# Kernel tuning notes

Measured on AMD Instinct MI355X. Metric: run time of the kernel, lower is better.

The kernel has to match this reference:

```python
import jax, jax.numpy as jnp
import numpy as np

N = 100000   # nodes
E = 5000000  # edges (avg degree 50)
H = 16       # hidden dim


def gcn_conv(x, edge_index, edge_weight, W, b, num_nodes):
    """PyG GCNConv with edge weights: add self-loops (weight 1), symmetric
    normalization deg^-1/2 * w * deg^-1/2, linear transform, scatter-add."""
    row, col = edge_index[0], edge_index[1]  # source j -> target i
    loop = jnp.arange(num_nodes, dtype=edge_index.dtype)
    row = jnp.concatenate([row, loop])
    col = jnp.concatenate([col, loop])
    w = jnp.concatenate([edge_weight, jnp.ones((num_nodes,), edge_weight.dtype)])
    deg = jax.ops.segment_sum(w, col, num_segments=num_nodes)
    dinv = jnp.where(deg > 0, jax.lax.rsqrt(jnp.where(deg > 0, deg, 1.0)), 0.0)
    norm = dinv[row] * w * dinv[col]               # [E+N]
    h = x @ W                                      # [N, out]
    msg = norm[:, None] * h[row]                   # gather + scale
    out = jax.ops.segment_sum(msg, col, num_segments=num_nodes)  # scatter-add
    return out + b


def setup_inputs() -> dict:
    key = jax.random.key(0)
    k = jax.random.split(key, 7)
    x = jax.random.normal(k[0], (N, 1), dtype=jnp.float32)
    edge_index = jax.random.randint(k[1], (2, E), 0, N, dtype=jnp.int32)
    edge_attr = jax.random.uniform(k[2], (E,), dtype=jnp.float32)
    W1 = jax.random.normal(k[3], (1, H), dtype=jnp.float32) * (1.0 / np.sqrt(1.0))
    b1 = jnp.zeros((H,), dtype=jnp.float32)
    W2 = jax.random.normal(k[4], (H, 1), dtype=jnp.float32) * (1.0 / np.sqrt(H))
    b2 = jnp.zeros((1,), dtype=jnp.float32)
    return {"x": x, "edge_index": edge_index, "edge_attr": edge_attr,
            "W1": W1, "b1": b1, "W2": W2, "b2": b2}


def reference(x, edge_index, edge_attr, W1, b1, W2, b2):
    h = gcn_conv(x, edge_index, edge_attr, W1, b1, N)
    h = jax.nn.relu(h)
    out = gcn_conv(h, edge_index, edge_attr, W2, b2, N)
    return out
```

## Files before the change

kernel.cpp:

```cpp
#include <hip/hip_runtime.h>

#define T       256
#define BSHIFT  12
#define BSIZE   4096
#define MAXNB   32
#define M       32
#define EPB     4096
#define EPT     (EPB / T)

__global__ void k_count(const int* __restrict__ col, int* __restrict__ cntT,
                        int E, int nb, int ebp) {
    __shared__ int hist[MAXNB];
    int t = threadIdx.x, g = blockIdx.x;
    if (t < MAXNB) hist[t] = 0;
    __syncthreads();
    int base = g * EPB;
    bool full = (base + EPB <= E);
    if (full) {
#pragma unroll
        for (int k = 0; k < EPT / 4; ++k) {
            int4 c = *(const int4*)(col + base + (t + k * T) * 4);
            atomicAdd(&hist[c.x >> BSHIFT], 1);
            atomicAdd(&hist[c.y >> BSHIFT], 1);
            atomicAdd(&hist[c.z >> BSHIFT], 1);
            atomicAdd(&hist[c.w >> BSHIFT], 1);
        }
    } else {
        for (int k = 0; k < EPT; ++k) {
            int e = base + t + k * T;
            if (e < E) atomicAdd(&hist[col[e] >> BSHIFT], 1);
        }
    }
    __syncthreads();
    if (t < nb) cntT[t * ebp + g] = hist[t];
}

__global__ void k_scan(const int* __restrict__ cntT, int* __restrict__ ofsT,
                       int* __restrict__ tot, int eb, int ebp) {
    __shared__ int tsum[T];
    __shared__ int carry;
    int b = blockIdx.x, t = threadIdx.x;
    if (t == 0) carry = 0;
    __syncthreads();
    int rounds = (eb + T - 1) / T;
    for (int jr = 0; jr < rounds; ++jr) {
        int idx = jr * T + t;
        int v = (idx < eb) ? cntT[b * ebp + idx] : 0;
        tsum[t] = v;
        __syncthreads();
        for (int d = 1; d < T; d <<= 1) {
            int o = (t >= d) ? tsum[t - d] : 0;
            __syncthreads();
            tsum[t] += o;
            __syncthreads();
        }
        int excl = tsum[t] - v + carry;
        if (idx < eb) ofsT[b * ebp + idx] = excl;
        __syncthreads();
        if (t == 0) carry += tsum[T - 1];
        __syncthreads();
    }
    if (t == 0) tot[b] = carry;
}

__global__ void k_scatter(const int* __restrict__ row, const int* __restrict__ col,
                          const float* __restrict__ w,
                          const int* __restrict__ cntT, const int* __restrict__ ofsT,
                          const int* __restrict__ tot,
                          int2* __restrict__ rec, int E, int nb, int ebp) {
    __shared__ int  lofs[MAXNB + 1];
    __shared__ int  rnk[MAXNB];
    __shared__ int  rbase[MAXNB];
    __shared__ int2 buf[EPB];
    __shared__ unsigned char bkt[EPB];
    int t = threadIdx.x, g = blockIdx.x;
    if (t < MAXNB) rnk[t] = 0;
    if (t < 64) {
        int tv = (t < nb) ? ((tot[t] + 3) & ~3) : 0;
        int incA = tv;
#pragma unroll
        for (int d = 1; d < 32; d <<= 1) {
            int o = __shfl_up(incA, d, 64);
            if (t >= d) incA += o;
        }
        int h = (t < nb) ? cntT[t * ebp + g] : 0;
        int incB = h;
#pragma unroll
        for (int d = 1; d < 32; d <<= 1) {
            int o = __shfl_up(incB, d, 64);
            if (t >= d) incB += o;
        }
        if (t == 0) lofs[0] = 0;
        if (t < nb) {
            lofs[t + 1] = incB;
            rbase[t] = (incA - tv) + ofsT[t * ebp + g];
        }
    }
    __syncthreads();

    int base = g * EPB;
    bool full = (base + EPB <= E);
    if (full) {
#pragma unroll
        for (int k = 0; k < EPT / 4; ++k) {
            int idx = base + (t + k * T) * 4;
            int4   c  = *(const int4*)(col + idx);
            int4   r  = *(const int4*)(row + idx);
            float4 wv = *(const float4*)(w + idx);
            int b, rk, pos;
            b = c.x >> BSHIFT; rk = atomicAdd(&rnk[b], 1); pos = lofs[b] + rk;
            buf[pos] = make_int2(((c.x & (BSIZE-1)) << 17) | r.x, __float_as_int(wv.x));
            bkt[pos] = (unsigned char)b;
            b = c.y >> BSHIFT; rk = atomicAdd(&rnk[b], 1); pos = lofs[b] + rk;
            buf[pos] = make_int2(((c.y & (BSIZE-1)) << 17) | r.y, __float_as_int(wv.y));
            bkt[pos] = (unsigned char)b;
            b = c.z >> BSHIFT; rk = atomicAdd(&rnk[b], 1); pos = lofs[b] + rk;
            buf[pos] = make_int2(((c.z & (BSIZE-1)) << 17) | r.z, __float_as_int(wv.z));
            bkt[pos] = (unsigned char)b;
            b = c.w >> BSHIFT; rk = atomicAdd(&rnk[b], 1); pos = lofs[b] + rk;
            buf[pos] = make_int2(((c.w & (BSIZE-1)) << 17) | r.w, __float_as_int(wv.w));
            bkt[pos] = (unsigned char)b;
        }
    } else {
        for (int k = 0; k < EPT; ++k) {
            int e = base + t + k * T;
            if (e < E) {
                int c = col[e];
                int b = c >> BSHIFT;
                int rk = atomicAdd(&rnk[b], 1);
                int pos = lofs[b] + rk;
                buf[pos] = make_int2(((c & (BSIZE-1)) << 17) | row[e], __float_as_int(w[e]));
                bkt[pos] = (unsigned char)b;
            }
        }
    }
    __syncthreads();
    int total = lofs[nb];
    for (int j = t; j < total; j += T) {
        int b = bkt[j];
        rec[rbase[b] + (j - lofs[b])] = buf[j];
    }
}

template <bool HAS_SRC>
__global__ void k_acc(const int2* __restrict__ rec, const int* __restrict__ tot,
                      const float* __restrict__ src, float* __restrict__ part, int nb) {
    __shared__ float acc[BSIZE];
    __shared__ int   bst[MAXNB];
    int t = threadIdx.x, g = blockIdx.x;
    int b = g / M, m = g % M;
    if (t < 64) {
        int tv = (t < nb) ? ((tot[t] + 3) & ~3) : 0;
        int inc = tv;
#pragma unroll
        for (int d = 1; d < 32; d <<= 1) {
            int o = __shfl_up(inc, d, 64);
            if (t >= d) inc += o;
        }
        if (t < nb) bst[t] = inc - tv;
    }
    for (int j = t; j < BSIZE; j += T) acc[j] = 0.0f;
    __syncthreads();
    int s  = bst[b];
    int tb = tot[b];
    int chunk = ((tb + M - 1) / M + 7) & ~7;
    int lo = s + m * chunk;
    int hi = min(s + tb, lo + chunk);
    const int4* rec4 = (const int4*)rec;
    int i = lo + t * 8;
    for (; i + 7 < hi; i += T * 8) {
        int4 q0 = rec4[(i >> 1) + 0];
        int4 q1 = rec4[(i >> 1) + 1];
        int4 q2 = rec4[(i >> 1) + 2];
        int4 q3 = rec4[(i >> 1) + 3];
        float v0 = __int_as_float(q0.y), v1 = __int_as_float(q0.w);
        float v2 = __int_as_float(q1.y), v3 = __int_as_float(q1.w);
        float v4 = __int_as_float(q2.y), v5 = __int_as_float(q2.w);
        float v6 = __int_as_float(q3.y), v7 = __int_as_float(q3.w);
        if (HAS_SRC) {
            v0 *= src[q0.x & 0x1FFFF]; v1 *= src[q0.z & 0x1FFFF];
            v2 *= src[q1.x & 0x1FFFF]; v3 *= src[q1.z & 0x1FFFF];
            v4 *= src[q2.x & 0x1FFFF]; v5 *= src[q2.z & 0x1FFFF];
            v6 *= src[q3.x & 0x1FFFF]; v7 *= src[q3.z & 0x1FFFF];
        }
        atomicAdd(&acc[((unsigned)q0.x) >> 17], v0);
        atomicAdd(&acc[((unsigned)q0.z) >> 17], v1);
        atomicAdd(&acc[((unsigned)q1.x) >> 17], v2);
        atomicAdd(&acc[((unsigned)q1.z) >> 17], v3);
        atomicAdd(&acc[((unsigned)q2.x) >> 17], v4);
        atomicAdd(&acc[((unsigned)q2.z) >> 17], v5);
        atomicAdd(&acc[((unsigned)q3.x) >> 17], v6);
        atomicAdd(&acc[((unsigned)q3.z) >> 17], v7);
    }
    for (; i < hi; ++i) {
        int2 r = rec[i];
        float v = __int_as_float(r.y);
        if (HAS_SRC) v *= src[r.x & 0x1FFFF];
        atomicAdd(&acc[((unsigned)r.x) >> 17], v);
    }
    __syncthreads();
    float* dst = part + (size_t)g * BSIZE;
    for (int j = t; j < BSIZE; j += T) dst[j] = acc[j];
}

__device__ __forceinline__ float reduceM(const float* __restrict__ part, int n) {
    int b = n >> BSHIFT, o = n & (BSIZE - 1);
    const float* pp = part + (size_t)b * M * BSIZE + o;
    float s = 0.0f;
#pragma unroll
    for (int m = 0; m < M; ++m) s += pp[(size_t)m * BSIZE];
    return s;
}

__global__ void k_red_dinv(const float* __restrict__ part, const float* __restrict__ x,
                           float* __restrict__ dinv, float* __restrict__ p, int N) {
    int i = blockIdx.x * blockDim.x + threadIdx.x;
    if (i < N) {
        float d  = reduceM(part, i) + 1.0f;
        float di = rsqrtf(d);
        dinv[i] = di;
        p[i] = di * x[i];
    }
}

__global__ void k_red_mlp(const float* __restrict__ part, const float* __restrict__ dinv,
                          const float* __restrict__ p,
                          const float* __restrict__ W1, const float* __restrict__ b1,
                          const float* __restrict__ W2,
                          float* __restrict__ q, int N) {
    int i = blockIdx.x * blockDim.x + threadIdx.x;
    if (i < N) {
        float di = dinv[i];
        float s  = di * reduceM(part, i) + di * p[i];
        float acc = 0.0f;
#pragma unroll
        for (int k = 0; k < 16; ++k) {
            float h = fmaxf(s * W1[k] + b1[k], 0.0f);
            acc += h * W2[k];
        }
        q[i] = di * acc;
    }
}

__global__ void k_red_out(const float* __restrict__ part, const float* __restrict__ dinv,
                          const float* __restrict__ q, const float* __restrict__ b2,
                          float* __restrict__ out, int N) {
    int i = blockIdx.x * blockDim.x + threadIdx.x;
    if (i < N) {
        float di = dinv[i];
        out[i] = di * reduceM(part, i) + di * q[i] + b2[0];
    }
}

extern "C" void kernel_launch(void* const* d_in, const int* in_sizes, int n_in,
                              void* d_out, int out_size, void* d_ws, size_t ws_size,
                              hipStream_t stream) {
    const float* x  = (const float*)d_in[0];
    const int*   ei = (const int*)  d_in[1];
    const float* ew = (const float*)d_in[2];
    const float* W1 = (const float*)d_in[3];
    const float* b1 = (const float*)d_in[4];
    const float* W2 = (const float*)d_in[5];
    const float* b2 = (const float*)d_in[6];

    const int N = in_sizes[0];
    const int E = in_sizes[2];
    const int* row = ei;
    const int* col = ei + E;
    const int nb  = (N + BSIZE - 1) >> BSHIFT;
    const int eb  = (E + EPB - 1) / EPB;
    const int ebp = (eb + 63) & ~63;

    char* wsp = (char*)d_ws;
    auto take = [&](size_t bytes) {
        char* r = wsp; wsp += (bytes + 255) & ~(size_t)255; return (void*)r;
    };
    int2*  rec  = (int2*) take((size_t)(E + 4 * MAXNB) * 8);
    float* part = (float*)take((size_t)nb * M * BSIZE * 4);
    float* dinv = (float*)take((size_t)N * 4);
    float* p    = (float*)take((size_t)N * 4);
    float* q    = (float*)take((size_t)N * 4);
    int*   cntT = (int*)  take((size_t)MAXNB * ebp * 4);
    int*   ofsT = (int*)  take((size_t)MAXNB * ebp * 4);
    int*   tot  = (int*)  take(MAXNB * 4);

    float* out = (float*)d_out;

    const int nbk = (N + T - 1) / T;
    const int ab  = nb * M;

    k_count  <<<eb, T, 0, stream>>>(col, cntT, E, nb, ebp);
    k_scan   <<<nb, T, 0, stream>>>(cntT, ofsT, tot, eb, ebp);
    k_scatter<<<eb, T, 0, stream>>>(row, col, ew, cntT, ofsT, tot, rec, E, nb, ebp);

    k_acc<false><<<ab, T, 0, stream>>>(rec, tot, nullptr, part, nb);
    k_red_dinv  <<<nbk, T, 0, stream>>>(part, x, dinv, p, N);

    k_acc<true><<<ab, T, 0, stream>>>(rec, tot, p, part, nb);
    k_red_mlp  <<<nbk, T, 0, stream>>>(part, dinv, p, W1, b1, W2, q, N);

    k_acc<true><<<ab, T, 0, stream>>>(rec, tot, q, part, nb);
    k_red_out  <<<nbk, T, 0, stream>>>(part, dinv, q, b2, out, N);
}
```

Baseline: 239.1 us.

## Use nontemporal loads/stores, warp-shuffle scan, vectorized zeroing, retune M and EPB

Marks streaming global loads and stores (edge arrays, bucketed records, partial sums) as nontemporal, swaps the shared-memory block scan for a wave-shuffle scan, and vectorizes accumulator zeroing and writeback. It also doubles the per-bucket split M and halves edges per scatter block to raise parallelism, and adds launch bounds. The larger M doubles the partial buffer and the per-node reduction work in the reduce kernels. The nontemporal hints may also hurt when the records are re-read by both accumulation passes.

After: 268.9 us. +12.5%, slower.

```diff
diff --git a/kernel.cpp b/kernel.cpp
--- a/kernel.cpp
+++ b/kernel.cpp
@@ -4,12 +4,17 @@
 #define BSHIFT  12
 #define BSIZE   4096
 #define MAXNB   32
-#define M       32
-#define EPB     4096
+#define M       64
+#define EPB     2048
 #define EPT     (EPB / T)
 
-__global__ void k_count(const int* __restrict__ col, int* __restrict__ cntT,
-                        int E, int nb, int ebp) {
+typedef int   i4 __attribute__((ext_vector_type(4)));
+typedef int   i2v __attribute__((ext_vector_type(2)));
+typedef float f4 __attribute__((ext_vector_type(4)));
+
+__global__ __launch_bounds__(T) void k_count(const int* __restrict__ col,
+                                             int* __restrict__ cntT,
+                                             int E, int nb, int ebp) {
     __shared__ int hist[MAXNB];
     int t = threadIdx.x, g = blockIdx.x;
     if (t < MAXNB) hist[t] = 0;
@@ -19,7 +24,7 @@
     if (full) {
 #pragma unroll
         for (int k = 0; k < EPT / 4; ++k) {
-            int4 c = *(const int4*)(col + base + (t + k * T) * 4);
+            i4 c = __builtin_nontemporal_load((const i4*)(col + base + (t + k * T) * 4));
             atomicAdd(&hist[c.x >> BSHIFT], 1);
             atomicAdd(&hist[c.y >> BSHIFT], 1);
             atomicAdd(&hist[c.z >> BSHIFT], 1);
@@ -35,43 +40,46 @@
     if (t < nb) cntT[t * ebp + g] = hist[t];
 }
 
-__global__ void k_scan(const int* __restrict__ cntT, int* __restrict__ ofsT,
-                       int* __restrict__ tot, int eb, int ebp) {
-    __shared__ int tsum[T];
+__global__ __launch_bounds__(T) void k_scan(const int* __restrict__ cntT,
+                                            int* __restrict__ ofsT,
+                                            int* __restrict__ tot, int eb, int ebp) {
+    __shared__ int wsum[4];
     __shared__ int carry;
-    int b = blockIdx.x, t = threadIdx.x;
+    int b = blockIdx.x, t = threadIdx.x, lane = t & 63, wid = t >> 6;
     if (t == 0) carry = 0;
     __syncthreads();
     int rounds = (eb + T - 1) / T;
     for (int jr = 0; jr < rounds; ++jr) {
         int idx = jr * T + t;
         int v = (idx < eb) ? cntT[b * ebp + idx] : 0;
-        tsum[t] = v;
+        int inc = v;
+#pragma unroll
+        for (int d = 1; d < 64; d <<= 1) {
+            int o = __shfl_up(inc, d, 64);
+            if (lane >= d) inc += o;
+        }
+        if (lane == 63) wsum[wid] = inc;
         __syncthreads();
-        for (int d = 1; d < T; d <<= 1) {
-            int o = (t >= d) ? tsum[t - d] : 0;
-            __syncthreads();
-            tsum[t] += o;
-            __syncthreads();
-        }
-        int excl = tsum[t] - v + carry;
-        if (idx < eb) ofsT[b * ebp + idx] = excl;
+        int add = carry;
+        for (int w = 0; w < wid; ++w) add += wsum[w];
+        if (idx < eb) ofsT[b * ebp + idx] = inc - v + add;
         __syncthreads();
-        if (t == 0) carry += tsum[T - 1];
+        if (t == 0) carry += wsum[0] + wsum[1] + wsum[2] + wsum[3];
         __syncthreads();
     }
     if (t == 0) tot[b] = carry;
 }
 
-__global__ void k_scatter(const int* __restrict__ row, const int* __restrict__ col,
-                          const float* __restrict__ w,
-                          const int* __restrict__ cntT, const int* __restrict__ ofsT,
-                          const int* __restrict__ tot,
-                          int2* __restrict__ rec, int E, int nb, int ebp) {
+__global__ __launch_bounds__(T) void k_scatter(
+        const int* __restrict__ row, const int* __restrict__ col,
+        const float* __restrict__ w,
+        const int* __restrict__ cntT, const int* __restrict__ ofsT,
+        const int* __restrict__ tot,
+        i2v* __restrict__ rec, int E, int nb, int ebp) {
     __shared__ int  lofs[MAXNB + 1];
     __shared__ int  rnk[MAXNB];
     __shared__ int  rbase[MAXNB];
-    __shared__ int2 buf[EPB];
+    __shared__ i2v  buf[EPB];
     __shared__ unsigned char bkt[EPB];
     int t = threadIdx.x, g = blockIdx.x;
     if (t < MAXNB) rnk[t] = 0;
@@ -104,22 +112,23 @@
 #pragma unroll
         for (int k = 0; k < EPT / 4; ++k) {
             int idx = base + (t + k * T) * 4;
-            int4   c  = *(const int4*)(col + idx);
-            int4   r  = *(const int4*)(row + idx);
-            float4 wv = *(const float4*)(w + idx);
+            i4 c  = __builtin_nontemporal_load((const i4*)(col + idx));
+            i4 r  = __builtin_nontemporal_load((const i4*)(row + idx));
+            f4 wv = __builtin_nontemporal_load((const f4*)(w + idx));
             int b, rk, pos;
+            i2v v;
             b = c.x >> BSHIFT; rk = atomicAdd(&rnk[b], 1); pos = lofs[b] + rk;
-            buf[pos] = make_int2(((c.x & (BSIZE-1)) << 17) | r.x, __float_as_int(wv.x));
-            bkt[pos] = (unsigned char)b;
+            v.x = ((c.x & (BSIZE-1)) << 17) | r.x; v.y = __float_as_int(wv.x);
+            buf[pos] = v; bkt[pos] = (unsigned char)b;
             b = c.y >> BSHIFT; rk = atomicAdd(&rnk[b], 1); pos = lofs[b] + rk;
-            buf[pos] = make_int2(((c.y & (BSIZE-1)) << 17) | r.y, __float_as_int(wv.y));
-            bkt[pos] = (unsigned char)b;
+            v.x = ((c.y & (BSIZE-1)) << 17) | r.y; v.y = __float_as_int(wv.y);
+            buf[pos] = v; bkt[pos] = (unsigned char)b;
             b = c.z >> BSHIFT; rk = atomicAdd(&rnk[b], 1); pos = lofs[b] + rk;
-            buf[pos] = make_int2(((c.z & (BSIZE-1)) << 17) | r.z, __float_as_int(wv.z));
-            bkt[pos] = (unsigned char)b;
+            v.x = ((c.z & (BSIZE-1)) << 17) | r.z; v.y = __float_as_int(wv.z);
+            buf[pos] = v; bkt[pos] = (unsigned char)b;
             b = c.w >> BSHIFT; rk = atomicAdd(&rnk[b], 1); pos = lofs[b] + rk;
-            buf[pos] = make_int2(((c.w & (BSIZE-1)) << 17) | r.w, __float_as_int(wv.w));
-            bkt[pos] = (unsigned char)b;
+            v.x = ((c.w & (BSIZE-1)) << 17) | r.w; v.y = __float_as_int(wv.w);
+            buf[pos] = v; bkt[pos] = (unsigned char)b;
         }
     } else {
         for (int k = 0; k < EPT; ++k) {
@@ -129,8 +138,10 @@
                 int b = c >> BSHIFT;
                 int rk = atomicAdd(&rnk[b], 1);
                 int pos = lofs[b] + rk;
-                buf[pos] = make_int2(((c & (BSIZE-1)) << 17) | row[e], __float_as_int(w[e]));
-                bkt[pos] = (unsigned char)b;
+                i2v v;
+                v.x = ((c & (BSIZE-1)) << 17) | row[e];
+                v.y = __float_as_int(w[e]);
+                buf[pos] = v; bkt[pos] = (unsigned char)b;
             }
         }
     }
@@ -138,13 +149,14 @@
     int total = lofs[nb];
     for (int j = t; j < total; j += T) {
         int b = bkt[j];
-        rec[rbase[b] + (j - lofs[b])] = buf[j];
+        __builtin_nontemporal_store(buf[j], &rec[rbase[b] + (j - lofs[b])]);
     }
 }
 
 template <bool HAS_SRC>
-__global__ void k_acc(const int2* __restrict__ rec, const int* __restrict__ tot,
-                      const float* __restrict__ src, float* __restrict__ part, int nb) {
+__global__ __launch_bounds__(T) void k_acc(
+        const i2v* __restrict__ rec, const int* __restrict__ tot,
+        const float* __restrict__ src, float* __restrict__ part, int nb) {
     __shared__ float acc[BSIZE];
     __shared__ int   bst[MAXNB];
     int t = threadIdx.x, g = blockIdx.x;
@@ -159,20 +171,21 @@
         }
         if (t < nb) bst[t] = inc - tv;
     }
-    for (int j = t; j < BSIZE; j += T) acc[j] = 0.0f;
+    f4* acc4 = (f4*)acc;
+    for (int j = t; j < BSIZE / 4; j += T) acc4[j] = (f4){0.f, 0.f, 0.f, 0.f};
     __syncthreads();
     int s  = bst[b];
     int tb = tot[b];
     int chunk = ((tb + M - 1) / M + 7) & ~7;
     int lo = s + m * chunk;
     int hi = min(s + tb, lo + chunk);
-    const int4* rec4 = (const int4*)rec;
+    const i4* rec4 = (const i4*)rec;
     int i = lo + t * 8;
     for (; i + 7 < hi; i += T * 8) {
-        int4 q0 = rec4[(i >> 1) + 0];
-        int4 q1 = rec4[(i >> 1) + 1];
-        int4 q2 = rec4[(i >> 1) + 2];
-        int4 q3 = rec4[(i >> 1) + 3];
+        i4 q0 = __builtin_nontemporal_load(rec4 + (i >> 1) + 0);
+        i4 q1 = __builtin_nontemporal_load(rec4 + (i >> 1) + 1);
+        i4 q2 = __builtin_nontemporal_load(rec4 + (i >> 1) + 2);
+        i4 q3 = __builtin_nontemporal_load(rec4 + (i >> 1) + 3);
         float v0 = __int_as_float(q0.y), v1 = __int_as_float(q0.w);
         float v2 = __int_as_float(q1.y), v3 = __int_as_float(q1.w);
         float v4 = __int_as_float(q2.y), v5 = __int_as_float(q2.w);
@@ -193,14 +206,15 @@
         atomicAdd(&acc[((unsigned)q3.z) >> 17], v7);
     }
     for (; i < hi; ++i) {
-        int2 r = rec[i];
+        i2v r = rec[i];
         float v = __int_as_float(r.y);
         if (HAS_SRC) v *= src[r.x & 0x1FFFF];
         atomicAdd(&acc[((unsigned)r.x) >> 17], v);
     }
     __syncthreads();
-    float* dst = part + (size_t)g * BSIZE;
-    for (int j = t; j < BSIZE; j += T) dst[j] = acc[j];
+    f4* dst4 = (f4*)(part + (size_t)g * BSIZE);
+    for (int j = t; j < BSIZE / 4; j += T)
+        __builtin_nontemporal_store(acc4[j], dst4 + j);
 }
 
 __device__ __forceinline__ float reduceM(const float* __restrict__ part, int n) {
@@ -208,7 +222,8 @@
     const float* pp = part + (size_t)b * M * BSIZE + o;
     float s = 0.0f;
 #pragma unroll
-    for (int m = 0; m < M; ++m) s += pp[(size_t)m * BSIZE];
+    for (int m = 0; m < M; ++m)
+        s += __builtin_nontemporal_load(pp + (size_t)m * BSIZE);
     return s;
 }
 
@@ -275,7 +290,7 @@
     auto take = [&](size_t bytes) {
         char* r = wsp; wsp += (bytes + 255) & ~(size_t)255; return (void*)r;
     };
-    int2*  rec  = (int2*) take((size_t)(E + 4 * MAXNB) * 8);
+    i2v*   rec  = (i2v*)  take((size_t)(E + 4 * MAXNB) * 8);
     float* part = (float*)take((size_t)nb * M * BSIZE * 4);
     float* dinv = (float*)take((size_t)N * 4);
     float* p    = (float*)take((size_t)N * 4);
```
